# Kernel optimization log

Measured on AMD Instinct MI355X. Metric: run time of the kernel, lower is better.

Reference implementation:

```python
import jax, jax.numpy as jnp
import numpy as np

B, TQ, TV = 16, 2048, 2048
DEC, ENC = 1024, 512

def setup_inputs() -> dict:
    key = jax.random.key(0)
    k1, k2, k3 = jax.random.split(key, 3)
    query = jax.random.normal(k1, (B, TQ, DEC), dtype=jnp.float32)
    value = jax.random.normal(k2, (B, TV, ENC), dtype=jnp.float32)
    # Dense(decoder_dim): kernel [ENC, DEC] + bias [DEC]
    W = jax.random.normal(k3, (ENC, DEC), dtype=jnp.float32) * (1.0 / np.sqrt(ENC))
    b = jnp.zeros((DEC,), dtype=jnp.float32)
    return {"query": query, "value": value, "W": W, "b": b}

def reference(query, value, W, b):
    # w(value): [B, TV, DEC]
    keys = jnp.einsum('bve,ed->bvd', value, W) + b
    # scores: query @ keys^T -> [B, TQ, TV]
    scores = jnp.einsum('bqd,bvd->bqv', query, keys)
    alignment = jax.nn.softmax(scores, axis=-1)
    # context: alignment @ value -> [B, TQ, ENC]
    context = jnp.einsum('bqv,bve->bqe', alignment, value)
    context = jnp.concatenate([context, query], axis=-1)  # [B, TQ, ENC+DEC]
    alignment_t = jnp.transpose(alignment, (0, 2, 1))      # [B, TV, TQ]
    return (context, alignment_t)
```

## Files before the change

### kernel.cpp

```cpp
#include <hip/hip_runtime.h>
#include <cstdint>
#include <cstddef>

typedef unsigned short u16;
typedef __bf16 bf16x8 __attribute__((ext_vector_type(8)));
typedef unsigned short u16x8 __attribute__((ext_vector_type(8)));
typedef unsigned short u16x4 __attribute__((ext_vector_type(4)));
typedef float f32x4 __attribute__((ext_vector_type(4)));

#define NB   16
#define TQ   2048
#define TV   2048
#define DDEC 1024
#define DENC 512
#define CTXW (DENC + DDEC)

#define ASTR 40

static __device__ __forceinline__ u16 f2bf(float f) {
    unsigned u = __builtin_bit_cast(unsigned, f);
    return (u16)((u + 0x7fffu + ((u >> 16) & 1u)) >> 16);
}
static __device__ __forceinline__ float bf2f(u16 h) {
    return __builtin_bit_cast(float, ((unsigned)h) << 16);
}

static __device__ __forceinline__ void stage_tile(
    u16* __restrict__ lds_tile, const u16* __restrict__ gsrc,
    int ldb, int w, int lane)
{
    #pragma unroll
    for (int p = 0; p < 2; ++p) {
        const int ci  = p * 4 + w;
        const int row = ci * 16 + (lane >> 2);
        const int col = (lane & 3) * 8;
        const u16* g = gsrc + (size_t)row * ldb + col;
        u16* l = lds_tile + ci * 512;
        __builtin_amdgcn_global_load_lds(
            (const __attribute__((address_space(1))) void*)g,
            (__attribute__((address_space(3))) void*)l, 16, 0, 0);
    }
}

__global__ __launch_bounds__(256)
void lk_prep_w(const float* __restrict__ W, u16* __restrict__ Wh, u16* __restrict__ Wl)
{
    const size_t i = ((size_t)blockIdx.x * 256 + threadIdx.x) * 4;
    const float4 v = *(const float4*)(W + i);
    const u16 h0=f2bf(v.x), h1=f2bf(v.y), h2=f2bf(v.z), h3=f2bf(v.w);
    u16x4 hv = {h0,h1,h2,h3};
    u16x4 lv = {f2bf(v.x-bf2f(h0)), f2bf(v.y-bf2f(h1)),
                f2bf(v.z-bf2f(h2)), f2bf(v.w-bf2f(h3))};
    *(u16x4*)(Wh + i) = hv;
    *(u16x4*)(Wl + i) = lv;
}

__global__ __launch_bounds__(256)
void lk_prep_v(const float* __restrict__ V, u16* __restrict__ Vh,
               u16* __restrict__ Vl, u16* __restrict__ Vt)
{
    __shared__ float ts[32][36];
    const int t = threadIdx.x;
    const int r = t >> 3, c = (t & 7) * 4;
    const int e0 = blockIdx.x * 32, v0 = blockIdx.y * 32;
    const size_t bin  = (size_t)blockIdx.z * TV * DENC;
    const float4 v = *(const float4*)(V + bin + (size_t)(v0 + r) * DENC + e0 + c);
    *(float4*)&ts[r][c] = v;
    const u16 h0=f2bf(v.x), h1=f2bf(v.y), h2=f2bf(v.z), h3=f2bf(v.w);
    u16x4 hv = {h0,h1,h2,h3};
    u16x4 lv = {f2bf(v.x-bf2f(h0)), f2bf(v.y-bf2f(h1)),
                f2bf(v.z-bf2f(h2)), f2bf(v.w-bf2f(h3))};
    *(u16x4*)(Vh + bin + (size_t)(v0 + r) * DENC + e0 + c) = hv;
    *(u16x4*)(Vl + bin + (size_t)(v0 + r) * DENC + e0 + c) = lv;
    __syncthreads();
    u16x4 tv;
    #pragma unroll
    for (int x = 0; x < 4; ++x) tv[x] = f2bf(ts[c + x][r]);
    *(u16x4*)(Vt + (size_t)blockIdx.z * DENC * TV + (size_t)(e0 + r) * TV + v0 + c) = tv;
}

__global__ __launch_bounds__(256)
void lk_gemm_qw(const float* __restrict__ A, const u16* __restrict__ Bh,
                const u16* __restrict__ Bl, u16* __restrict__ Chi,
                u16* __restrict__ Clo)
{
    __shared__ u16 lAh[128*ASTR], lAl[128*ASTR], lBh[128*32], lBl[128*32];
    const int m0 = blockIdx.x * 128, n0 = blockIdx.y * 128;
    const int t = threadIdx.x;
    const int w = t >> 6, lane = t & 63, l15 = lane & 15, quad = lane >> 4;

    f32x4 acc[2][8];
    #pragma unroll
    for (int i = 0; i < 2; ++i)
        #pragma unroll
        for (int j = 0; j < 8; ++j) acc[i][j] = (f32x4){0.f,0.f,0.f,0.f};

    const int ar = t >> 3, ac = (t & 7) * 4;

    for (int k0 = 0; k0 < DDEC; k0 += 32) {
        stage_tile(lBh, Bh + (size_t)n0 * DDEC + k0, DDEC, w, lane);
        stage_tile(lBl, Bl + (size_t)n0 * DDEC + k0, DDEC, w, lane);
        #pragma unroll
        for (int it = 0; it < 4; ++it) {
            const int r = ar + it * 32;
            const float4 v = *(const float4*)(A + (size_t)(m0 + r) * DDEC + k0 + ac);
            const u16 h0=f2bf(v.x), h1=f2bf(v.y), h2=f2bf(v.z), h3=f2bf(v.w);
            u16x4 hv = {h0,h1,h2,h3};
            u16x4 lv = {f2bf(v.x-bf2f(h0)), f2bf(v.y-bf2f(h1)),
                        f2bf(v.z-bf2f(h2)), f2bf(v.w-bf2f(h3))};
            *(u16x4*)&lAh[r*ASTR+ac] = hv;
            *(u16x4*)&lAl[r*ASTR+ac] = lv;
        }
        __syncthreads();
        bf16x8 ah[2], al[2];
        #pragma unroll
        for (int tm = 0; tm < 2; ++tm) {
            const int row = w*32 + tm*16 + l15;
            ah[tm] = __builtin_bit_cast(bf16x8, *(const u16x8*)&lAh[row*ASTR + quad*8]);
            al[tm] = __builtin_bit_cast(bf16x8, *(const u16x8*)&lAl[row*ASTR + quad*8]);
        }
        #pragma unroll
        for (int tn = 0; tn < 8; ++tn) {
            const int col = tn*16 + l15;
            const bf16x8 bh = __builtin_bit_cast(bf16x8, *(const u16x8*)&lBh[col*32 + quad*8]);
            const bf16x8 bl = __builtin_bit_cast(bf16x8, *(const u16x8*)&lBl[col*32 + quad*8]);
            #pragma unroll
            for (int tm = 0; tm < 2; ++tm) {
                acc[tm][tn] = __builtin_amdgcn_mfma_f32_16x16x32_bf16(ah[tm], bh, acc[tm][tn], 0,0,0);
                acc[tm][tn] = __builtin_amdgcn_mfma_f32_16x16x32_bf16(ah[tm], bl, acc[tm][tn], 0,0,0);
                acc[tm][tn] = __builtin_amdgcn_mfma_f32_16x16x32_bf16(al[tm], bh, acc[tm][tn], 0,0,0);
            }
        }
        __syncthreads();
    }
    #pragma unroll
    for (int tn = 0; tn < 8; ++tn) {
        const int col = n0 + tn*16 + l15;
        #pragma unroll
        for (int tm = 0; tm < 2; ++tm)
            #pragma unroll
            for (int r = 0; r < 4; ++r) {
                const int row = m0 + w*32 + tm*16 + quad*4 + r;
                const float c = acc[tm][tn][r];
                const u16 h = f2bf(c);
                Chi[(size_t)row*DENC + col] = h;
                Clo[(size_t)row*DENC + col] = f2bf(c - bf2f(h));
            }
    }
}

__global__ __launch_bounds__(256)
void lk_gemm_scores(const u16* __restrict__ Ah_g, const u16* __restrict__ Al_g,
                    const u16* __restrict__ Bh_g, const u16* __restrict__ Bl_g,
                    float* __restrict__ Sc)
{
    __shared__ u16 lAh[128*32], lAl[128*32], lBh[128*32], lBl[128*32];
    const int b = blockIdx.z;
    const int m0 = blockIdx.x * 128, n0 = blockIdx.y * 128;
    const int t = threadIdx.x;
    const int w = t >> 6, lane = t & 63, l15 = lane & 15, quad = lane >> 4;

    const u16* Ab_h = Ah_g + (size_t)b * TQ * DENC + (size_t)m0 * DENC;
    const u16* Ab_l = Al_g + (size_t)b * TQ * DENC + (size_t)m0 * DENC;
    const u16* Bb_h = Bh_g + (size_t)b * TV * DENC + (size_t)n0 * DENC;
    const u16* Bb_l = Bl_g + (size_t)b * TV * DENC + (size_t)n0 * DENC;

    f32x4 acc[2][8];
    #pragma unroll
    for (int i = 0; i < 2; ++i)
        #pragma unroll
        for (int j = 0; j < 8; ++j) acc[i][j] = (f32x4){0.f,0.f,0.f,0.f};

    for (int k0 = 0; k0 < DENC; k0 += 32) {
        stage_tile(lAh, Ab_h + k0, DENC, w, lane);
        stage_tile(lAl, Ab_l + k0, DENC, w, lane);
        stage_tile(lBh, Bb_h + k0, DENC, w, lane);
        stage_tile(lBl, Bb_l + k0, DENC, w, lane);
        __syncthreads();
        bf16x8 ah[2], al[2];
        #pragma unroll
        for (int tm = 0; tm < 2; ++tm) {
            const int row = w*32 + tm*16 + l15;
            ah[tm] = __builtin_bit_cast(bf16x8, *(const u16x8*)&lAh[row*32 + quad*8]);
            al[tm] = __builtin_bit_cast(bf16x8, *(const u16x8*)&lAl[row*32 + quad*8]);
        }
        #pragma unroll
        for (int tn = 0; tn < 8; ++tn) {
            const int col = tn*16 + l15;
            const bf16x8 bh = __builtin_bit_cast(bf16x8, *(const u16x8*)&lBh[col*32 + quad*8]);
            const bf16x8 bl = __builtin_bit_cast(bf16x8, *(const u16x8*)&lBl[col*32 + quad*8]);
            #pragma unroll
            for (int tm = 0; tm < 2; ++tm) {
                acc[tm][tn] = __builtin_amdgcn_mfma_f32_16x16x32_bf16(ah[tm], bh, acc[tm][tn], 0,0,0);
                acc[tm][tn] = __builtin_amdgcn_mfma_f32_16x16x32_bf16(ah[tm], bl, acc[tm][tn], 0,0,0);
                acc[tm][tn] = __builtin_amdgcn_mfma_f32_16x16x32_bf16(al[tm], bh, acc[tm][tn], 0,0,0);
            }
        }
        __syncthreads();
    }
    float* Sb = Sc + (size_t)b * TQ * TV;
    #pragma unroll
    for (int tm = 0; tm < 2; ++tm)
        #pragma unroll
        for (int tn = 0; tn < 8; ++tn) {
            const int col = n0 + tn*16 + l15;
            #pragma unroll
            for (int r = 0; r < 4; ++r) {
                const int row = m0 + w*32 + tm*16 + quad*4 + r;
                Sb[(size_t)row*TV + col] = acc[tm][tn][r];
            }
        }
}

__global__ __launch_bounds__(256)
void lk_softmax(float* __restrict__ S)
{
    float* p = S + (size_t)blockIdx.x * TV;
    const int t = threadIdx.x;
    const float4 v0 = *(const float4*)(p + 4*t);
    const float4 v1 = *(const float4*)(p + 1024 + 4*t);
    float mx = fmaxf(fmaxf(fmaxf(v0.x, v0.y), fmaxf(v0.z, v0.w)),
                     fmaxf(fmaxf(v1.x, v1.y), fmaxf(v1.z, v1.w)));
    #pragma unroll
    for (int off = 32; off > 0; off >>= 1) mx = fmaxf(mx, __shfl_xor(mx, off, 64));
    __shared__ float sred[4];
    const int w = t >> 6;
    if ((t & 63) == 0) sred[w] = mx;
    __syncthreads();
    mx = fmaxf(fmaxf(sred[0], sred[1]), fmaxf(sred[2], sred[3]));
    __syncthreads();
    float e[8];
    e[0]=__expf(v0.x-mx); e[1]=__expf(v0.y-mx); e[2]=__expf(v0.z-mx); e[3]=__expf(v0.w-mx);
    e[4]=__expf(v1.x-mx); e[5]=__expf(v1.y-mx); e[6]=__expf(v1.z-mx); e[7]=__expf(v1.w-mx);
    float s = ((e[0]+e[1])+(e[2]+e[3])) + ((e[4]+e[5])+(e[6]+e[7]));
    #pragma unroll
    for (int off = 32; off > 0; off >>= 1) s += __shfl_xor(s, off, 64);
    if ((t & 63) == 0) sred[w] = s;
    __syncthreads();
    s = (sred[0]+sred[1]) + (sred[2]+sred[3]);
    const float inv = 1.0f / s;
    float4 o0 = {e[0]*inv, e[1]*inv, e[2]*inv, e[3]*inv};
    float4 o1 = {e[4]*inv, e[5]*inv, e[6]*inv, e[7]*inv};
    *(float4*)(p + 4*t) = o0;
    *(float4*)(p + 1024 + 4*t) = o1;
}

__global__ __launch_bounds__(256)
void lk_gemm_ctx(const float* __restrict__ P, const u16* __restrict__ Vt,
                 float* __restrict__ C)
{
    __shared__ u16 lA[128*ASTR], lB[128*32];
    const int b = blockIdx.z;
    const int m0 = blockIdx.x * 128, n0 = blockIdx.y * 128;
    const int t = threadIdx.x;
    const int w = t >> 6, lane = t & 63, l15 = lane & 15, quad = lane >> 4;

    const float* Pb = P + (size_t)b * TQ * TV;
    const u16* Bb = Vt + (size_t)b * DENC * TV + (size_t)n0 * TV;

    f32x4 acc[2][8];
    #pragma unroll
    for (int i = 0; i < 2; ++i)
        #pragma unroll
        for (int j = 0; j < 8; ++j) acc[i][j] = (f32x4){0.f,0.f,0.f,0.f};

    const int ar = t >> 3, ac = (t & 7) * 4;

    for (int k0 = 0; k0 < TV; k0 += 32) {
        stage_tile(lB, Bb + k0, TV, w, lane);
        #pragma unroll
        for (int it = 0; it < 4; ++it) {
            const int r = ar + it * 32;
            const float4 v = *(const float4*)(Pb + (size_t)(m0 + r) * TV + k0 + ac);
            u16x4 hv = {f2bf(v.x), f2bf(v.y), f2bf(v.z), f2bf(v.w)};
            *(u16x4*)&lA[r*ASTR+ac] = hv;
        }
        __syncthreads();
        bf16x8 af[2];
        #pragma unroll
        for (int tm = 0; tm < 2; ++tm) {
            const int row = w*32 + tm*16 + l15;
            af[tm] = __builtin_bit_cast(bf16x8, *(const u16x8*)&lA[row*ASTR + quad*8]);
        }
        #pragma unroll
        for (int tn = 0; tn < 8; ++tn) {
            const int col = tn*16 + l15;
            const bf16x8 bf = __builtin_bit_cast(bf16x8, *(const u16x8*)&lB[col*32 + quad*8]);
            #pragma unroll
            for (int tm = 0; tm < 2; ++tm)
                acc[tm][tn] = __builtin_amdgcn_mfma_f32_16x16x32_bf16(af[tm], bf, acc[tm][tn], 0,0,0);
        }
        __syncthreads();
    }
    float* Cb = C + (size_t)b * TQ * CTXW;
    #pragma unroll
    for (int tm = 0; tm < 2; ++tm)
        #pragma unroll
        for (int tn = 0; tn < 8; ++tn) {
            const int col = n0 + tn*16 + l15;
            #pragma unroll
            for (int r = 0; r < 4; ++r) {
                const int row = m0 + w*32 + tm*16 + quad*4 + r;
                Cb[(size_t)row*CTXW + col] = acc[tm][tn][r];
            }
        }
}

__global__ __launch_bounds__(256)
void lk_copy_q(const float* __restrict__ Q, float* __restrict__ C)
{
    const size_t idx = (size_t)blockIdx.x * 256 + threadIdx.x;
    const int d4 = (int)(idx & 255);
    const size_t row = idx >> 8;
    const float4 v = *(const float4*)(Q + (row << 10) + 4*d4);
    *(float4*)(C + row * CTXW + DENC + 4*d4) = v;
}

__global__ __launch_bounds__(256)
void lk_transpose(float* __restrict__ A)
{
    const int i = blockIdx.x, j = blockIdx.y;
    if (j < i) return;
    float* Ab = A + (size_t)blockIdx.z * TQ * TV;
    __shared__ float ta[32][36], tb[32][36];
    const int t = threadIdx.x;
    const int r = t >> 3, c = (t & 7) * 4;
    float* pij = Ab + (size_t)(i*32) * TV + j*32;
    float* pji = Ab + (size_t)(j*32) * TV + i*32;
    const float4 va = *(const float4*)(pij + (size_t)r * TV + c);
    *(float4*)&ta[r][c] = va;
    if (i != j) {
        const float4 vb = *(const float4*)(pji + (size_t)r * TV + c);
        *(float4*)&tb[r][c] = vb;
    }
    __syncthreads();
    float4 oa = { ta[c+0][r], ta[c+1][r], ta[c+2][r], ta[c+3][r] };
    *(float4*)(pji + (size_t)r * TV + c) = oa;
    if (i != j) {
        float4 ob = { tb[c+0][r], tb[c+1][r], tb[c+2][r], tb[c+3][r] };
        *(float4*)(pij + (size_t)r * TV + c) = ob;
    }
}

extern "C" void kernel_launch(void* const* d_in, const int* in_sizes, int n_in,
                              void* d_out, int out_size, void* d_ws, size_t ws_size,
                              hipStream_t stream)
{
    (void)in_sizes; (void)n_in; (void)out_size; (void)ws_size;
    const float* Q = (const float*)d_in[0];
    const float* V = (const float*)d_in[1];
    const float* W = (const float*)d_in[2];
    float* out = (float*)d_out;

    float* ctx   = out;
    float* align = out + (size_t)NB * TQ * CTXW;

    u16* q2h = (u16*)ctx;
    u16* q2l = q2h + (size_t)NB * TQ * DENC;
    u16* vsh = q2l + (size_t)NB * TQ * DENC;
    u16* vsl = vsh + (size_t)NB * TV * DENC;

    u16* wh = (u16*)d_ws;
    u16* wl = wh + (size_t)DENC * DDEC;
    u16* vt = wl + (size_t)DENC * DDEC;

    lk_prep_w<<<DENC*DDEC/1024, 256, 0, stream>>>(W, wh, wl);
    lk_prep_v<<<dim3(DENC/32, TV/32, NB), 256, 0, stream>>>(V, vsh, vsl, vt);
    lk_gemm_qw<<<dim3(NB*TQ/128, DENC/128), 256, 0, stream>>>(Q, wh, wl, q2h, q2l);
    lk_gemm_scores<<<dim3(TQ/128, TV/128, NB), 256, 0, stream>>>(q2h, q2l, vsh, vsl, align);
    lk_softmax<<<NB*TQ, 256, 0, stream>>>(align);
    lk_gemm_ctx<<<dim3(TQ/128, DENC/128, NB), 256, 0, stream>>>(align, vt, ctx);
    lk_copy_q<<<NB*TQ*DDEC/1024, 256, 0, stream>>>(Q, ctx);
    lk_transpose<<<dim3(TV/32, TV/32, NB), 256, 0, stream>>>(align);
}
```

Before: 1.497 ms.

## Pre-convert Q and softmax probabilities to bf16 for async LDS staging

A new pass splits Q into bf16 hi/lo arrays, stored in the unused alignment buffer. The softmax also writes a bf16 copy of the probabilities into the query slots of the context output. The two GEMMs can then stage both operands with global_load_lds instead of loading fp32, converting in registers and writing LDS by hand, which also halves the bytes the context GEMM reads for P. The trade-offs are an extra full pass over Q, and unpadded LDS rows that may cause bank conflicts on the fragment reads.

```diff
diff --git a/kernel.cpp b/kernel.cpp
--- a/kernel.cpp
+++ b/kernel.cpp
@@ -14,8 +14,7 @@
 #define DDEC 1024
 #define DENC 512
 #define CTXW (DENC + DDEC)
-
-#define ASTR 40
+#define CTXW2 (2*CTXW)
 
 static __device__ __forceinline__ u16 f2bf(float f) {
     unsigned u = __builtin_bit_cast(unsigned, f);
@@ -43,16 +42,16 @@
 }
 
 __global__ __launch_bounds__(256)
-void lk_prep_w(const float* __restrict__ W, u16* __restrict__ Wh, u16* __restrict__ Wl)
+void lk_prep_split(const float* __restrict__ X, u16* __restrict__ Xh, u16* __restrict__ Xl)
 {
     const size_t i = ((size_t)blockIdx.x * 256 + threadIdx.x) * 4;
-    const float4 v = *(const float4*)(W + i);
+    const float4 v = *(const float4*)(X + i);
     const u16 h0=f2bf(v.x), h1=f2bf(v.y), h2=f2bf(v.z), h3=f2bf(v.w);
     u16x4 hv = {h0,h1,h2,h3};
     u16x4 lv = {f2bf(v.x-bf2f(h0)), f2bf(v.y-bf2f(h1)),
                 f2bf(v.z-bf2f(h2)), f2bf(v.w-bf2f(h3))};
-    *(u16x4*)(Wh + i) = hv;
-    *(u16x4*)(Wl + i) = lv;
+    *(u16x4*)(Xh + i) = hv;
+    *(u16x4*)(Xl + i) = lv;
 }
 
 __global__ __launch_bounds__(256)
@@ -80,44 +79,38 @@
 }
 
 __global__ __launch_bounds__(256)
-void lk_gemm_qw(const float* __restrict__ A, const u16* __restrict__ Bh,
-                const u16* __restrict__ Bl, u16* __restrict__ Chi,
-                u16* __restrict__ Clo)
-{
-    __shared__ u16 lAh[128*ASTR], lAl[128*ASTR], lBh[128*32], lBl[128*32];
+void lk_gemm_qw(const u16* __restrict__ Ah_g, const u16* __restrict__ Al_g,
+                const u16* __restrict__ Bh_g, const u16* __restrict__ Bl_g,
+                u16* __restrict__ Chi, u16* __restrict__ Clo)
+{
+    __shared__ u16 lAh[128*32], lAl[128*32], lBh[128*32], lBl[128*32];
     const int m0 = blockIdx.x * 128, n0 = blockIdx.y * 128;
     const int t = threadIdx.x;
     const int w = t >> 6, lane = t & 63, l15 = lane & 15, quad = lane >> 4;
 
+    const u16* Ab_h = Ah_g + (size_t)m0 * DDEC;
+    const u16* Ab_l = Al_g + (size_t)m0 * DDEC;
+    const u16* Bb_h = Bh_g + (size_t)n0 * DDEC;
+    const u16* Bb_l = Bl_g + (size_t)n0 * DDEC;
+
     f32x4 acc[2][8];
     #pragma unroll
     for (int i = 0; i < 2; ++i)
         #pragma unroll
         for (int j = 0; j < 8; ++j) acc[i][j] = (f32x4){0.f,0.f,0.f,0.f};
 
-    const int ar = t >> 3, ac = (t & 7) * 4;
-
     for (int k0 = 0; k0 < DDEC; k0 += 32) {
-        stage_tile(lBh, Bh + (size_t)n0 * DDEC + k0, DDEC, w, lane);
-        stage_tile(lBl, Bl + (size_t)n0 * DDEC + k0, DDEC, w, lane);
-        #pragma unroll
-        for (int it = 0; it < 4; ++it) {
-            const int r = ar + it * 32;
-            const float4 v = *(const float4*)(A + (size_t)(m0 + r) * DDEC + k0 + ac);
-            const u16 h0=f2bf(v.x), h1=f2bf(v.y), h2=f2bf(v.z), h3=f2bf(v.w);
-            u16x4 hv = {h0,h1,h2,h3};
-            u16x4 lv = {f2bf(v.x-bf2f(h0)), f2bf(v.y-bf2f(h1)),
-                        f2bf(v.z-bf2f(h2)), f2bf(v.w-bf2f(h3))};
-            *(u16x4*)&lAh[r*ASTR+ac] = hv;
-            *(u16x4*)&lAl[r*ASTR+ac] = lv;
-        }
+        stage_tile(lAh, Ab_h + k0, DDEC, w, lane);
+        stage_tile(lAl, Ab_l + k0, DDEC, w, lane);
+        stage_tile(lBh, Bb_h + k0, DDEC, w, lane);
+        stage_tile(lBl, Bb_l + k0, DDEC, w, lane);
         __syncthreads();
         bf16x8 ah[2], al[2];
         #pragma unroll
         for (int tm = 0; tm < 2; ++tm) {
             const int row = w*32 + tm*16 + l15;
-            ah[tm] = __builtin_bit_cast(bf16x8, *(const u16x8*)&lAh[row*ASTR + quad*8]);
-            al[tm] = __builtin_bit_cast(bf16x8, *(const u16x8*)&lAl[row*ASTR + quad*8]);
+            ah[tm] = __builtin_bit_cast(bf16x8, *(const u16x8*)&lAh[row*32 + quad*8]);
+            al[tm] = __builtin_bit_cast(bf16x8, *(const u16x8*)&lAl[row*32 + quad*8]);
         }
         #pragma unroll
         for (int tn = 0; tn < 8; ++tn) {
@@ -213,9 +206,11 @@
 }
 
 __global__ __launch_bounds__(256)
-void lk_softmax(float* __restrict__ S)
-{
-    float* p = S + (size_t)blockIdx.x * TV;
+void lk_softmax(float* __restrict__ S, u16* __restrict__ Pbf)
+{
+    const size_t row = blockIdx.x;
+    float* p = S + row * TV;
+    u16* pb = Pbf + row * CTXW2 + 2*DENC;
     const int t = threadIdx.x;
     const float4 v0 = *(const float4*)(p + 4*t);
     const float4 v1 = *(const float4*)(p + 1024 + 4*t);
@@ -243,19 +238,22 @@
     float4 o1 = {e[4]*inv, e[5]*inv, e[6]*inv, e[7]*inv};
     *(float4*)(p + 4*t) = o0;
     *(float4*)(p + 1024 + 4*t) = o1;
-}
-
-__global__ __launch_bounds__(256)
-void lk_gemm_ctx(const float* __restrict__ P, const u16* __restrict__ Vt,
-                 float* __restrict__ C)
-{
-    __shared__ u16 lA[128*ASTR], lB[128*32];
+    u16x4 b0 = {f2bf(o0.x), f2bf(o0.y), f2bf(o0.z), f2bf(o0.w)};
+    u16x4 b1 = {f2bf(o1.x), f2bf(o1.y), f2bf(o1.z), f2bf(o1.w)};
+    *(u16x4*)(pb + 4*t) = b0;
+    *(u16x4*)(pb + 1024 + 4*t) = b1;
+}
+
+__global__ __launch_bounds__(256)
+void lk_gemm_ctx(const u16* __restrict__ Vt, float* C)
+{
+    __shared__ u16 lA[128*32], lB[128*32];
     const int b = blockIdx.z;
     const int m0 = blockIdx.x * 128, n0 = blockIdx.y * 128;
     const int t = threadIdx.x;
     const int w = t >> 6, lane = t & 63, l15 = lane & 15, quad = lane >> 4;
 
-    const float* Pb = P + (size_t)b * TQ * TV;
+    const u16* Pb = (const u16*)C + ((size_t)b * TQ + m0) * CTXW2 + 2*DENC;
     const u16* Bb = Vt + (size_t)b * DENC * TV + (size_t)n0 * TV;
 
     f32x4 acc[2][8];
@@ -264,23 +262,15 @@
         #pragma unroll
         for (int j = 0; j < 8; ++j) acc[i][j] = (f32x4){0.f,0.f,0.f,0.f};
 
-    const int ar = t >> 3, ac = (t & 7) * 4;
-
     for (int k0 = 0; k0 < TV; k0 += 32) {
+        stage_tile(lA, Pb + k0, CTXW2, w, lane);
         stage_tile(lB, Bb + k0, TV, w, lane);
-        #pragma unroll
-        for (int it = 0; it < 4; ++it) {
-            const int r = ar + it * 32;
-            const float4 v = *(const float4*)(Pb + (size_t)(m0 + r) * TV + k0 + ac);
-            u16x4 hv = {f2bf(v.x), f2bf(v.y), f2bf(v.z), f2bf(v.w)};
-            *(u16x4*)&lA[r*ASTR+ac] = hv;
-        }
         __syncthreads();
         bf16x8 af[2];
         #pragma unroll
         for (int tm = 0; tm < 2; ++tm) {
             const int row = w*32 + tm*16 + l15;
-            af[tm] = __builtin_bit_cast(bf16x8, *(const u16x8*)&lA[row*ASTR + quad*8]);
+            af[tm] = __builtin_bit_cast(bf16x8, *(const u16x8*)&lA[row*32 + quad*8]);
         }
         #pragma unroll
         for (int tn = 0; tn < 8; ++tn) {
@@ -360,16 +350,20 @@
     u16* vsh = q2l + (size_t)NB * TQ * DENC;
     u16* vsl = vsh + (size_t)NB * TV * DENC;
 
+    u16* qh = (u16*)align;
+    u16* ql = qh + (size_t)NB * TQ * DDEC;
+
     u16* wh = (u16*)d_ws;
     u16* wl = wh + (size_t)DENC * DDEC;
     u16* vt = wl + (size_t)DENC * DDEC;
 
-    lk_prep_w<<<DENC*DDEC/1024, 256, 0, stream>>>(W, wh, wl);
+    lk_prep_split<<<DENC*DDEC/1024, 256, 0, stream>>>(W, wh, wl);
+    lk_prep_split<<<(size_t)NB*TQ*DDEC/1024, 256, 0, stream>>>(Q, qh, ql);
     lk_prep_v<<<dim3(DENC/32, TV/32, NB), 256, 0, stream>>>(V, vsh, vsl, vt);
-    lk_gemm_qw<<<dim3(NB*TQ/128, DENC/128), 256, 0, stream>>>(Q, wh, wl, q2h, q2l);
+    lk_gemm_qw<<<dim3(NB*TQ/128, DENC/128), 256, 0, stream>>>(qh, ql, wh, wl, q2h, q2l);
     lk_gemm_scores<<<dim3(TQ/128, TV/128, NB), 256, 0, stream>>>(q2h, q2l, vsh, vsl, align);
-    lk_softmax<<<NB*TQ, 256, 0, stream>>>(align);
-    lk_gemm_ctx<<<dim3(TQ/128, DENC/128, NB), 256, 0, stream>>>(align, vt, ctx);
+    lk_softmax<<<NB*TQ, 256, 0, stream>>>(align, (u16*)ctx);
+    lk_gemm_ctx<<<dim3(TQ/128, DENC/128, NB), 256, 0, stream>>>(vt, ctx);
     lk_copy_q<<<NB*TQ*DDEC/1024, 256, 0, stream>>>(Q, ctx);
     lk_transpose<<<dim3(TV/32, TV/32, NB), 256, 0, stream>>>(align);
 }
```

Result: faster. 1.334 ms (-10.9%).
